# Performance work log

Hardware: AMD Instinct MI355X
Metric: run time of the kernel (lower is better)

## Reference

```python
import jax, jax.numpy as jnp
import numpy as np

NUM_CLASSES = 2
KS = 5  # kernel_size
EPS = 1e-8  # torch cosine_similarity eps


def setup_inputs() -> dict:
    key = jax.random.key(0)
    k1, k2, k3 = jax.random.split(key, 3)
    b, c, h, w = 8, 256, 128, 128
    er_input = jax.random.normal(k1, (b, c, h, w), dtype=jnp.float32)
    seg_label = jax.random.randint(k2, (b, h, w), 0, 2, dtype=jnp.int32)
    gt_boundary_seg = jax.random.randint(k3, (b, h, w), 0, 2, dtype=jnp.int32)
    return {"er_input": er_input, "seg_label": seg_label, "gt_boundary_seg": gt_boundary_seg}


def _context_loss(er_input, seg_label, gt_boundary_seg):
    # seg_label / gt_boundary_seg already at er_input spatial size (nearest interp is identity)
    b, c, h, w = er_input.shape
    r = KS // 2
    seg0 = jnp.where(seg_label == 255, 0, seg_label)
    gtb0 = jnp.where(gt_boundary_seg == 255, 0, gt_boundary_seg)
    gt_b = gtb0 * seg0                                  # [b,h,w] boundary pixels on fg classes
    interior = jnp.zeros((h, w), bool).at[r:h - r, r:w - r].set(True)
    valid = (gt_b > 0) & interior                       # pixels whose 5x5 window is in-bounds
    include = (gt_b > 0).any(axis=(1, 2))               # images contributing to scale_num
    cnt = valid.sum(axis=(1, 2)).astype(er_input.dtype)  # [b]

    norm = jnp.maximum(jnp.sqrt((er_input * er_input).sum(axis=1)), EPS)  # [b,h,w]
    validf = valid.astype(er_input.dtype)
    total = jnp.zeros((b,), dtype=er_input.dtype)
    n_shift = 0
    for dy in range(-r, r + 1):
        for dx in range(-r, r + 1):
            if dy == 0 and dx == 0:
                continue
            n_shift += 1
            # value at p+ (dy,dx) brought to p; valid pixels are interior so no wrap issue
            feat_s = jnp.roll(er_input, (-dy, -dx), axis=(2, 3))
            norm_s = jnp.roll(norm, (-dy, -dx), axis=(1, 2))
            seg_s = jnp.roll(seg_label, (-dy, -dx), axis=(1, 2))
            dot = (er_input * feat_s).sum(axis=1)       # [b,h,w]
            cos = dot / (norm * norm_s)
            # one_hot(seg,256)[:num_classes] dot product == labels equal AND label < num_classes
            labsim = ((seg_label == seg_s) & (seg_label < NUM_CLASSES)).astype(er_input.dtype)
            sq = (cos - labsim) ** 2
            # mse_loss over selected boundary pixels of image i
            total = total + (sq * validf).sum(axis=(1, 2)) / jnp.maximum(cnt, 1.0)
    loss_i = total / float(n_shift)                     # per-image context_loss_pi / 24
    scale_num = jnp.maximum(include.sum(), 1)
    return (loss_i * include.astype(loss_i.dtype)).sum() / scale_num.astype(loss_i.dtype)


def reference(er_input, seg_label, gt_boundary_seg):
    return _context_loss(er_input, seg_label, gt_boundary_seg)
```

## Files before the change

### kernel.cpp

```cpp
#include <hip/hip_runtime.h>
#include <math.h>

#define BATCH 8
#define CH    256
#define H     128
#define W     128
#define PLANE (H * W)
#define NPIX  (BATCH * PLANE)
#define NSHIFT 12
#define NCHUNK 4
#define CPC    (CH / NCHUNK)

static __device__ __constant__ int S_DY[NSHIFT] = {0,0,1,1,1,1,1,2,2,2,2,2};
static __device__ __constant__ int S_DX[NSHIFT] = {1,2,-2,-1,0,1,2,-2,-1,0,1,2};

static __device__ __constant__ int P_DY[13] = {0,0,0,1,1,1,1,1,2,2,2,2,2};
static __device__ __constant__ int P_DX[13] = {0,1,2,-2,-1,0,1,2,-2,-1,0,1,2};

#define NZERO4 ((13 * NPIX + 32) / 4)

__global__ __launch_bounds__(256) void k_zero(float4* __restrict__ p) {
    int i = blockIdx.x * 256 + threadIdx.x;
    if (i < NZERO4) p[i] = make_float4(0.f, 0.f, 0.f, 0.f);
}

__global__ __launch_bounds__(256) void k_stats(const int* __restrict__ seg,
                                               const int* __restrict__ gtb,
                                               int* __restrict__ cnt,
                                               int* __restrict__ inc) {
    int b = blockIdx.x >> 6;
    int i = (blockIdx.x & 63) * 256 + threadIdx.x;
    int my_cnt = 0, my_any = 0;
    {
        int s = seg[b * PLANE + i];
        int g = gtb[b * PLANE + i];
        int s0 = (s == 255) ? 0 : s;
        int g0 = (g == 255) ? 0 : g;
        if (s0 > 0 && g0 > 0) {
            my_any = 1;
            int y = i >> 7, x = i & 127;
            if (y >= 2 && y < H - 2 && x >= 2 && x < W - 2) my_cnt = 1;
        }
    }
    for (int o = 32; o > 0; o >>= 1) {
        my_cnt += __shfl_down(my_cnt, o, 64);
        my_any |= __shfl_down(my_any, o, 64);
    }
    __shared__ int sc[4], sa[4];
    int lane = threadIdx.x & 63, wid = threadIdx.x >> 6;
    if (lane == 0) { sc[wid] = my_cnt; sa[wid] = my_any; }
    __syncthreads();
    if (threadIdx.x == 0) {
        int c = sc[0] + sc[1] + sc[2] + sc[3];
        int a = sa[0] | sa[1] | sa[2] | sa[3];
        if (c) atomicAdd(&cnt[b], c);
        if (a) atomicOr(&inc[b], 1);
    }
}

__global__ void k_factor(const int* __restrict__ cnt, const int* __restrict__ inc,
                         float* __restrict__ factor, float* __restrict__ out) {
    if (blockIdx.x == 0 && threadIdx.x == 0) {
        int sn = 0;
        for (int b = 0; b < BATCH; b++) sn += (inc[b] != 0);
        if (sn < 1) sn = 1;
        for (int b = 0; b < BATCH; b++) {
            int c = cnt[b] < 1 ? 1 : cnt[b];
            factor[b] = inc[b] ? 1.0f / (24.0f * (float)c * (float)sn) : 0.0f;
        }
        out[0] = 0.0f;
    }
}

__global__ __launch_bounds__(256) void k_corr(const float* __restrict__ er,
                                              float* __restrict__ dots,
                                              float* __restrict__ normsq) {
    __shared__ float4 lds[4][132];
    int blk = blockIdx.x;
    int chunk = blk & 3;
    int tile  = (blk >> 2) & 63;
    int b     = blk >> 8;
    int y0 = tile * 2;
    int c0 = chunk * CPC;
    int t = threadIdx.x;
    int r = t >> 7;
    int x = t & 127;

    if (t < 16) {
        int row = t >> 2, col = t & 3;
        int xs = (col < 2) ? col : (col + 128);
        lds[row][xs] = make_float4(0.f, 0.f, 0.f, 0.f);
    }

    float acc[13];
#pragma unroll
    for (int i = 0; i < 13; i++) acc[i] = 0.0f;

    const float* base = er + (size_t)b * CH * PLANE;

    for (int c = c0; c < c0 + CPC; c += 4) {
        __syncthreads();
#pragma unroll
        for (int k = 0; k < 2; ++k) {
            int s = t + k * 256;
            int row = s >> 7;
            int xs = s & 127;
            int y = y0 + row;
            float4 v = make_float4(0.f, 0.f, 0.f, 0.f);
            if (y < H) {
                const float* p0 = base + (size_t)c * PLANE + y * W + xs;
                v.x = p0[0];
                v.y = p0[PLANE];
                v.z = p0[2 * PLANE];
                v.w = p0[3 * PLANE];
            }
            lds[row][xs + 2] = v;
        }
        __syncthreads();

        const float4* lp = &lds[r][x + 2];
        float4 cen = lp[0];
#pragma unroll
        for (int i = 0; i < 13; ++i) {
            float4 v = lp[P_DY[i] * 132 + P_DX[i]];
            acc[i] = fmaf(cen.x, v.x, acc[i]);
            acc[i] = fmaf(cen.y, v.y, acc[i]);
            acc[i] = fmaf(cen.z, v.z, acc[i]);
            acc[i] = fmaf(cen.w, v.w, acc[i]);
        }
    }

    int y = y0 + r;
    int pix = b * PLANE + y * W + x;
    atomicAdd(&normsq[pix], acc[0]);
#pragma unroll
    for (int i = 0; i < NSHIFT; ++i)
        atomicAdd(&dots[i * NPIX + pix], acc[i + 1]);
}

__global__ __launch_bounds__(256) void k_loss(const float* __restrict__ dots,
                                              const float* __restrict__ normsq,
                                              const int* __restrict__ seg,
                                              const int* __restrict__ gtb,
                                              const float* __restrict__ factor,
                                              float* __restrict__ out) {
    int idx = blockIdx.x * 256 + threadIdx.x;
    int b = idx >> 14;
    int rem = idx & (PLANE - 1);
    int y = rem >> 7;
    int x = rem & 127;

    float val = 0.0f;
    if (y >= 2 && y < H - 2 && x >= 2 && x < W - 2) {
        int sp = seg[idx];
        int gp = gtb[idx];
        int s0 = (sp == 255) ? 0 : sp;
        int g0 = (gp == 255) ? 0 : gp;
        if (s0 > 0 && g0 > 0) {
            float np = fmaxf(sqrtf(normsq[idx]), 1e-8f);
            float sum = 0.0f;
#pragma unroll
            for (int i = 0; i < NSHIFT; ++i) {
                int off = S_DY[i] * W + S_DX[i];
                {
                    float d  = dots[i * NPIX + idx];
                    float nn = fmaxf(sqrtf(normsq[idx + off]), 1e-8f);
                    float cosv = d / (np * nn);
                    int sq = seg[idx + off];
                    float lab = (sp == sq && sp < 2) ? 1.0f : 0.0f;
                    float tt = cosv - lab;
                    sum = fmaf(tt, tt, sum);
                }
                {
                    float d  = dots[i * NPIX + idx - off];
                    float nn = fmaxf(sqrtf(normsq[idx - off]), 1e-8f);
                    float cosv = d / (np * nn);
                    int sq = seg[idx - off];
                    float lab = (sp == sq && sp < 2) ? 1.0f : 0.0f;
                    float tt = cosv - lab;
                    sum = fmaf(tt, tt, sum);
                }
            }
            val = sum * factor[b];
        }
    }

    for (int o = 32; o > 0; o >>= 1)
        val += __shfl_down(val, o, 64);
    __shared__ float wsum[4];
    int lane = threadIdx.x & 63;
    int wid  = threadIdx.x >> 6;
    if (lane == 0) wsum[wid] = val;
    __syncthreads();
    if (threadIdx.x == 0) {
        float s = wsum[0] + wsum[1] + wsum[2] + wsum[3];
        atomicAdd(out, s);
    }
}

extern "C" void kernel_launch(void* const* d_in, const int* in_sizes, int n_in,
                              void* d_out, int out_size, void* d_ws, size_t ws_size,
                              hipStream_t stream) {
    const float* er  = (const float*)d_in[0];
    const int*   seg = (const int*)d_in[1];
    const int*   gtb = (const int*)d_in[2];
    float* out = (float*)d_out;

    float* ws     = (float*)d_ws;
    float* dots   = ws;
    float* normsq = dots + NSHIFT * NPIX;
    float* factor = normsq + NPIX;
    int*   cnt    = (int*)(factor + 8);
    int*   inc    = cnt + 8;

    hipLaunchKernelGGL(k_zero,   dim3((NZERO4 + 255) / 256), dim3(256), 0, stream,
                       (float4*)d_ws);
    hipLaunchKernelGGL(k_stats,  dim3(BATCH * 64), dim3(256), 0, stream, seg, gtb, cnt, inc);
    hipLaunchKernelGGL(k_factor, dim3(1), dim3(64), 0, stream, cnt, inc, factor, out);
    hipLaunchKernelGGL(k_corr,   dim3(BATCH * 64 * NCHUNK), dim3(256), 0, stream,
                       er, dots, normsq);
    hipLaunchKernelGGL(k_loss,   dim3(NPIX / 256), dim3(256), 0, stream,
                       dots, normsq, seg, gtb, factor, out);
}
```

Measured before the change: 235.2 us.

## Compute two output rows per thread in corr and fold stats/factor into other kernels

Each correlation block now covers four rows instead of two. Every thread accumulates dot products for two vertically adjacent pixels, so neighbour values loaded from LDS are reused across both, and the halo reload per channel group drops from 2x to 1.5x. The stats reduction runs as extra blocks inside the correlation launch. The factor kernel is removed and each loss thread computes the per-image scaling inline, which cuts the launch count from five to three. The cost is twice as many accumulator registers per thread and half as many correlation blocks.

```diff
diff --git a/kernel.cpp b/kernel.cpp
--- a/kernel.cpp
+++ b/kernel.cpp
@@ -14,94 +14,94 @@
 static __device__ __constant__ int S_DY[NSHIFT] = {0,0,1,1,1,1,1,2,2,2,2,2};
 static __device__ __constant__ int S_DX[NSHIFT] = {1,2,-2,-1,0,1,2,-2,-1,0,1,2};
 
-static __device__ __constant__ int P_DY[13] = {0,0,0,1,1,1,1,1,2,2,2,2,2};
-static __device__ __constant__ int P_DX[13] = {0,1,2,-2,-1,0,1,2,-2,-1,0,1,2};
-
-#define NZERO4 ((13 * NPIX + 32) / 4)
-
-__global__ __launch_bounds__(256) void k_zero(float4* __restrict__ p) {
+#define NZERO4 ((13 * NPIX + 16) / 4)
+#define NZB    ((NZERO4 + 255) / 256)
+
+#define NCORRB (BATCH * 32 * NCHUNK)
+#define NSTATB (BATCH * 64)
+
+__device__ __forceinline__ void fma4(float& acc, const float4& a, const float4& b) {
+    acc = fmaf(a.x, b.x, acc);
+    acc = fmaf(a.y, b.y, acc);
+    acc = fmaf(a.z, b.z, acc);
+    acc = fmaf(a.w, b.w, acc);
+}
+
+__global__ __launch_bounds__(256) void k_prep(float4* __restrict__ p,
+                                              float* __restrict__ out) {
     int i = blockIdx.x * 256 + threadIdx.x;
     if (i < NZERO4) p[i] = make_float4(0.f, 0.f, 0.f, 0.f);
-}
-
-__global__ __launch_bounds__(256) void k_stats(const int* __restrict__ seg,
-                                               const int* __restrict__ gtb,
-                                               int* __restrict__ cnt,
-                                               int* __restrict__ inc) {
-    int b = blockIdx.x >> 6;
-    int i = (blockIdx.x & 63) * 256 + threadIdx.x;
-    int my_cnt = 0, my_any = 0;
-    {
-        int s = seg[b * PLANE + i];
-        int g = gtb[b * PLANE + i];
-        int s0 = (s == 255) ? 0 : s;
-        int g0 = (g == 255) ? 0 : g;
-        if (s0 > 0 && g0 > 0) {
-            my_any = 1;
-            int y = i >> 7, x = i & 127;
-            if (y >= 2 && y < H - 2 && x >= 2 && x < W - 2) my_cnt = 1;
-        }
-    }
-    for (int o = 32; o > 0; o >>= 1) {
-        my_cnt += __shfl_down(my_cnt, o, 64);
-        my_any |= __shfl_down(my_any, o, 64);
-    }
-    __shared__ int sc[4], sa[4];
-    int lane = threadIdx.x & 63, wid = threadIdx.x >> 6;
-    if (lane == 0) { sc[wid] = my_cnt; sa[wid] = my_any; }
-    __syncthreads();
-    if (threadIdx.x == 0) {
-        int c = sc[0] + sc[1] + sc[2] + sc[3];
-        int a = sa[0] | sa[1] | sa[2] | sa[3];
-        if (c) atomicAdd(&cnt[b], c);
-        if (a) atomicOr(&inc[b], 1);
-    }
-}
-
-__global__ void k_factor(const int* __restrict__ cnt, const int* __restrict__ inc,
-                         float* __restrict__ factor, float* __restrict__ out) {
-    if (blockIdx.x == 0 && threadIdx.x == 0) {
-        int sn = 0;
-        for (int b = 0; b < BATCH; b++) sn += (inc[b] != 0);
-        if (sn < 1) sn = 1;
-        for (int b = 0; b < BATCH; b++) {
-            int c = cnt[b] < 1 ? 1 : cnt[b];
-            factor[b] = inc[b] ? 1.0f / (24.0f * (float)c * (float)sn) : 0.0f;
-        }
-        out[0] = 0.0f;
-    }
+    if (i == 0) out[0] = 0.0f;
 }
 
 __global__ __launch_bounds__(256) void k_corr(const float* __restrict__ er,
+                                              const int* __restrict__ seg,
+                                              const int* __restrict__ gtb,
                                               float* __restrict__ dots,
-                                              float* __restrict__ normsq) {
-    __shared__ float4 lds[4][132];
+                                              float* __restrict__ normsq,
+                                              int* __restrict__ cnt,
+                                              int* __restrict__ inc) {
+    __shared__ float4 lds[6][132];
+    int t = threadIdx.x;
+
+    if (blockIdx.x >= NCORRB) {
+        int blk2 = blockIdx.x - NCORRB;
+        int b = blk2 >> 6;
+        int i = (blk2 & 63) * 256 + t;
+        int my_cnt = 0, my_any = 0;
+        {
+            int s = seg[b * PLANE + i];
+            int g = gtb[b * PLANE + i];
+            int s0 = (s == 255) ? 0 : s;
+            int g0 = (g == 255) ? 0 : g;
+            if (s0 > 0 && g0 > 0) {
+                my_any = 1;
+                int y = i >> 7, x = i & 127;
+                if (y >= 2 && y < H - 2 && x >= 2 && x < W - 2) my_cnt = 1;
+            }
+        }
+        for (int o = 32; o > 0; o >>= 1) {
+            my_cnt += __shfl_down(my_cnt, o, 64);
+            my_any |= __shfl_down(my_any, o, 64);
+        }
+        __shared__ int sc[4], sa[4];
+        int lane = t & 63, wid = t >> 6;
+        if (lane == 0) { sc[wid] = my_cnt; sa[wid] = my_any; }
+        __syncthreads();
+        if (t == 0) {
+            int c = sc[0] + sc[1] + sc[2] + sc[3];
+            int a = sa[0] | sa[1] | sa[2] | sa[3];
+            if (c) atomicAdd(&cnt[b], c);
+            if (a) atomicOr(&inc[b], 1);
+        }
+        return;
+    }
+
     int blk = blockIdx.x;
     int chunk = blk & 3;
-    int tile  = (blk >> 2) & 63;
-    int b     = blk >> 8;
-    int y0 = tile * 2;
+    int tile  = (blk >> 2) & 31;
+    int b     = blk >> 7;
+    int y0 = tile * 4;
     int c0 = chunk * CPC;
-    int t = threadIdx.x;
     int r = t >> 7;
     int x = t & 127;
 
-    if (t < 16) {
+    if (t < 24) {
         int row = t >> 2, col = t & 3;
         int xs = (col < 2) ? col : (col + 128);
         lds[row][xs] = make_float4(0.f, 0.f, 0.f, 0.f);
     }
 
-    float acc[13];
-#pragma unroll
-    for (int i = 0; i < 13; i++) acc[i] = 0.0f;
+    float accA[13], accB[13];
+#pragma unroll
+    for (int i = 0; i < 13; i++) { accA[i] = 0.0f; accB[i] = 0.0f; }
 
     const float* base = er + (size_t)b * CH * PLANE;
 
     for (int c = c0; c < c0 + CPC; c += 4) {
         __syncthreads();
 #pragma unroll
-        for (int k = 0; k < 2; ++k) {
+        for (int k = 0; k < 3; ++k) {
             int s = t + k * 256;
             int row = s >> 7;
             int xs = s & 127;
@@ -118,37 +118,79 @@
         }
         __syncthreads();
 
-        const float4* lp = &lds[r][x + 2];
-        float4 cen = lp[0];
-#pragma unroll
-        for (int i = 0; i < 13; ++i) {
-            float4 v = lp[P_DY[i] * 132 + P_DX[i]];
-            acc[i] = fmaf(cen.x, v.x, acc[i]);
-            acc[i] = fmaf(cen.y, v.y, acc[i]);
-            acc[i] = fmaf(cen.z, v.z, acc[i]);
-            acc[i] = fmaf(cen.w, v.w, acc[i]);
-        }
-    }
-
-    int y = y0 + r;
-    int pix = b * PLANE + y * W + x;
-    atomicAdd(&normsq[pix], acc[0]);
-#pragma unroll
-    for (int i = 0; i < NSHIFT; ++i)
-        atomicAdd(&dots[i * NPIX + pix], acc[i + 1]);
+        const float4* lp = &lds[2 * r][x + 2];
+        float4 cA = lp[0];
+        float4 cB = lp[132];
+        {
+            float4 v1 = lp[1], v2 = lp[2];
+            fma4(accA[0], cA, cA);
+            fma4(accA[1], cA, v1);
+            fma4(accA[2], cA, v2);
+        }
+        {
+            float4 m2 = lp[130], m1 = lp[131], p1 = lp[133], p2 = lp[134];
+            fma4(accA[3], cA, m2);
+            fma4(accA[4], cA, m1);
+            fma4(accA[5], cA, cB);
+            fma4(accA[6], cA, p1);
+            fma4(accA[7], cA, p2);
+            fma4(accB[0], cB, cB);
+            fma4(accB[1], cB, p1);
+            fma4(accB[2], cB, p2);
+        }
+        {
+            float4 m2 = lp[262], m1 = lp[263], v0 = lp[264], p1 = lp[265], p2 = lp[266];
+            fma4(accA[8],  cA, m2);
+            fma4(accA[9],  cA, m1);
+            fma4(accA[10], cA, v0);
+            fma4(accA[11], cA, p1);
+            fma4(accA[12], cA, p2);
+            fma4(accB[3], cB, m2);
+            fma4(accB[4], cB, m1);
+            fma4(accB[5], cB, v0);
+            fma4(accB[6], cB, p1);
+            fma4(accB[7], cB, p2);
+        }
+        {
+            float4 m2 = lp[394], m1 = lp[395], v0 = lp[396], p1 = lp[397], p2 = lp[398];
+            fma4(accB[8],  cB, m2);
+            fma4(accB[9],  cB, m1);
+            fma4(accB[10], cB, v0);
+            fma4(accB[11], cB, p1);
+            fma4(accB[12], cB, p2);
+        }
+    }
+
+    int pixA = b * PLANE + (y0 + 2 * r) * W + x;
+    int pixB = pixA + W;
+    atomicAdd(&normsq[pixA], accA[0]);
+    atomicAdd(&normsq[pixB], accB[0]);
+#pragma unroll
+    for (int i = 0; i < NSHIFT; ++i) {
+        atomicAdd(&dots[i * NPIX + pixA], accA[i + 1]);
+        atomicAdd(&dots[i * NPIX + pixB], accB[i + 1]);
+    }
 }
 
 __global__ __launch_bounds__(256) void k_loss(const float* __restrict__ dots,
                                               const float* __restrict__ normsq,
                                               const int* __restrict__ seg,
                                               const int* __restrict__ gtb,
-                                              const float* __restrict__ factor,
+                                              const int* __restrict__ cnt,
+                                              const int* __restrict__ inc,
                                               float* __restrict__ out) {
     int idx = blockIdx.x * 256 + threadIdx.x;
     int b = idx >> 14;
     int rem = idx & (PLANE - 1);
     int y = rem >> 7;
     int x = rem & 127;
+
+    int sn = 0;
+#pragma unroll
+    for (int b2 = 0; b2 < BATCH; b2++) sn += (inc[b2] != 0);
+    if (sn < 1) sn = 1;
+    int cb = cnt[b]; if (cb < 1) cb = 1;
+    float factor = inc[b] ? 1.0f / (24.0f * (float)cb * (float)sn) : 0.0f;
 
     float val = 0.0f;
     if (y >= 2 && y < H - 2 && x >= 2 && x < W - 2) {
@@ -181,7 +223,7 @@
                     sum = fmaf(tt, tt, sum);
                 }
             }
-            val = sum * factor[b];
+            val = sum * factor;
         }
     }
 
@@ -209,16 +251,12 @@
     float* ws     = (float*)d_ws;
     float* dots   = ws;
     float* normsq = dots + NSHIFT * NPIX;
-    float* factor = normsq + NPIX;
-    int*   cnt    = (int*)(factor + 8);
+    int*   cnt    = (int*)(normsq + NPIX);
     int*   inc    = cnt + 8;
 
-    hipLaunchKernelGGL(k_zero,   dim3((NZERO4 + 255) / 256), dim3(256), 0, stream,
-                       (float4*)d_ws);
-    hipLaunchKernelGGL(k_stats,  dim3(BATCH * 64), dim3(256), 0, stream, seg, gtb, cnt, inc);
-    hipLaunchKernelGGL(k_factor, dim3(1), dim3(64), 0, stream, cnt, inc, factor, out);
-    hipLaunchKernelGGL(k_corr,   dim3(BATCH * 64 * NCHUNK), dim3(256), 0, stream,
-                       er, dots, normsq);
-    hipLaunchKernelGGL(k_loss,   dim3(NPIX / 256), dim3(256), 0, stream,
-                       dots, normsq, seg, gtb, factor, out);
-}
+    hipLaunchKernelGGL(k_prep, dim3(NZB), dim3(256), 0, stream, (float4*)d_ws, out);
+    hipLaunchKernelGGL(k_corr, dim3(NCORRB + NSTATB), dim3(256), 0, stream,
+                       er, seg, gtb, dots, normsq, cnt, inc);
+    hipLaunchKernelGGL(k_loss, dim3(NPIX / 256), dim3(256), 0, stream,
+                       dots, normsq, seg, gtb, cnt, inc, out);
+}
```

Measured after the change: 230.4 us. -2.0%, faster.
